# Performance work log

Measured on AMD Instinct MI355X. Metric: run time of the kernel, lower is better.

## Reference

```python
import jax, jax.numpy as jnp
import numpy as np

C = 256
CK = C // 8  # qk projection dim


def setup_inputs() -> dict:
    key = jax.random.key(0)
    ks = jax.random.split(key, 8)
    B, H, W = 4, 64, 64
    x = jax.random.normal(ks[0], (B, C, W, H), dtype=jnp.float32)
    s = 1.0 / np.sqrt(C)
    Wf = jax.random.normal(ks[1], (CK, C), dtype=jnp.float32) * s
    bf = jax.random.normal(ks[2], (CK,), dtype=jnp.float32) * 0.01
    Wg = jax.random.normal(ks[3], (CK, C), dtype=jnp.float32) * s
    bg = jax.random.normal(ks[4], (CK,), dtype=jnp.float32) * 0.01
    Wh = jax.random.normal(ks[5], (C, C), dtype=jnp.float32) * s
    bh = jax.random.normal(ks[6], (C,), dtype=jnp.float32) * 0.01
    gamma = jax.random.normal(ks[7], (1,), dtype=jnp.float32) * 0.1
    return {"x": x, "Wf": Wf, "bf": bf, "Wg": Wg, "bg": bg,
            "Wh": Wh, "bh": bh, "gamma": gamma}


def reference(x, Wf, bf, Wg, bg, Wh, bh, gamma):
    B, Cc, Wd, Hd = x.shape
    N = Wd * Hd
    xf = x.reshape(B, Cc, N)  # B C N
    # 1x1 conv1d == channel matmul
    f = jnp.einsum('oc,bcn->bon', Wf, xf) + bf[None, :, None]  # B CK N
    g = jnp.einsum('oc,bcn->bon', Wg, xf) + bg[None, :, None]  # B CK N
    h = jnp.einsum('oc,bcn->bon', Wh, xf) + bh[None, :, None]  # B C N
    # s[b,i,j] = sum_k f[b,k,i] g[b,k,j]
    s = jnp.einsum('bki,bkj->bij', f, g)  # B N N
    attention = jax.nn.softmax(s, axis=-1)
    # out[b,c,i] = sum_j h[b,c,j] attention[b,i,j]
    out = jnp.einsum('bcj,bij->bci', h, attention)  # B C N
    out = out.reshape(B, Cc, Wd, Hd)
    return gamma[0] * out + x
```

## Files before the change

kernel.cpp:

```cpp
#include <hip/hip_runtime.h>

typedef __bf16 bf16x8 __attribute__((ext_vector_type(8)));
typedef __bf16 bf16x4 __attribute__((ext_vector_type(4)));
typedef float f32x4 __attribute__((ext_vector_type(4)));
typedef float f32x16 __attribute__((ext_vector_type(16)));

__device__ __forceinline__ f32x4 mfma16(bf16x8 a, bf16x8 b, f32x4 c) {
  return __builtin_amdgcn_mfma_f32_16x16x32_bf16(a, b, c, 0, 0, 0);
}
__device__ __forceinline__ f32x16 mfma32(bf16x8 a, bf16x8 b, f32x16 c) {
  return __builtin_amdgcn_mfma_f32_32x32x16_bf16(a, b, c, 0, 0, 0);
}

__global__ void wcvt_kernel(const float* __restrict__ Wf, const float* __restrict__ Wg,
                            const float* __restrict__ Wh, __bf16* __restrict__ Wb) {
  int i = blockIdx.x * 256 + threadIdx.x;
  float v;
  if (i < 8192)       v = Wf[i];
  else if (i < 16384) v = Wg[i - 8192];
  else                v = Wh[i - 16384];
  Wb[i] = (__bf16)v;
}

__global__ __launch_bounds__(512) void proj_kernel(
    const float* __restrict__ x, const float* __restrict__ bfv,
    const float* __restrict__ bgv, const float* __restrict__ bhv,
    const __bf16* __restrict__ Wb, __bf16* __restrict__ fgT,
    __bf16* __restrict__ hb) {
  __shared__ __align__(16) char smem[2560 + 18432];
  __bf16* xT = (__bf16*)smem;
  __bf16* ho = (__bf16*)(smem + 2560);

  const int t = threadIdx.x;
  const int l = t & 63, wg = t >> 6, q = l >> 4, l15 = l & 15;
  const int nh = wg & 1, oh = wg >> 1;
  const int bi = blockIdx.x;
  const int b = bi >> 7;
  const int n0 = (bi & 127) << 5;

  const float* xb = x + (size_t)b * 256 * 4096;

  f32x4 acc[5];
#pragma unroll
  for (int i = 0; i < 5; i++) acc[i] = (f32x4){0.f, 0.f, 0.f, 0.f};

  const int c_rel = t >> 4;
  const int n2 = (t & 15) * 2;

#pragma unroll 1
  for (int kc = 0; kc < 8; kc++) {
    __syncthreads();
    float2 v = *(const float2*)(xb + (size_t)(kc * 32 + c_rel) * 4096 + n0 + n2);
    xT[(n2 + 0) * 40 + c_rel] = (__bf16)v.x;
    xT[(n2 + 1) * 40 + c_rel] = (__bf16)v.y;
    __syncthreads();
    bf16x8 af = *(const bf16x8*)(xT + (nh * 16 + l15) * 40 + q * 8);
    const __bf16* wp = Wb + (size_t)(oh * 80 + l15) * 256 + kc * 32 + q * 8;
#pragma unroll
    for (int ot = 0; ot < 5; ot++) {
      bf16x8 bfr = *(const bf16x8*)(wp + (size_t)ot * 16 * 256);
      acc[ot] = mfma16(af, bfr, acc[ot]);
    }
  }

#pragma unroll
  for (int ot = 0; ot < 5; ot++) {
    int o = oh * 80 + ot * 16 + l15;
    float bias = (o < 32) ? bfv[o] : (o < 64) ? bgv[o - 32] : bhv[o - 64];
#pragma unroll
    for (int r = 0; r < 4; r++) {
      int n_rel = nh * 16 + q * 4 + r;
      float val = acc[ot][r] + bias;
      if (o < 64) {
        fgT[((size_t)b * 4096 + n0 + n_rel) * 64 + o] = (__bf16)val;
      } else {
        ho[(o - 64) * 36 + n_rel] = (__bf16)val;
      }
    }
  }
  __syncthreads();
  unsigned short* hbu = (unsigned short*)hb + (size_t)b * 256 * 4096 + n0;
  const unsigned short* hou = (const unsigned short*)ho;
  for (int e = t; e < 4096; e += 512) {
    int c = e >> 4, nn = (e & 15) * 2;
    unsigned int vv = *(const unsigned int*)(hou + c * 36 + nn);
    *(unsigned int*)(hbu + (size_t)c * 4096 + nn) = vv;
  }
}

__global__ __launch_bounds__(256, 3) void attn_kernel(
    const __bf16* __restrict__ fgT, const __bf16* __restrict__ hb,
    __bf16* __restrict__ pO, float* __restrict__ Lp) {
  __shared__ __align__(16) char smem[35072];
  __bf16* pb0 = (__bf16*)smem;
  __bf16* pb1 = (__bf16*)(smem + 17408);
  __bf16* stage = (__bf16*)smem;
  float* Lbuf = (float*)(smem + 34816);

  const int t = threadIdx.x;
  const int l = t & 63, w = t >> 6;
  const int h = l >> 5, l31 = l & 31;

  const int bi = blockIdx.x;
  const int xcd = bi & 7, slot = bi >> 3;
  const int combo = xcd * 2 + (slot & 1);
  const int b = combo >> 2, jp = combo & 3;
  const int n0 = (slot >> 1) << 6;

  const __bf16* fgb = fgT + (size_t)b * 4096 * 64;
  const __bf16* hbb = hb + (size_t)b * 256 * 4096;
  const int jq0 = jp << 10;

  if (t < 64) Lbuf[t] = 0.f;

  const int it_s = w >> 1, jt = w & 1;

  const __bf16* qp = fgb + (size_t)(n0 + it_s * 32 + l31) * 64 + h * 8;
  const bf16x8 qf0 = *(const bf16x8*)(qp);
  const bf16x8 qf1 = *(const bf16x8*)(qp + 16);

  f32x16 acc[2][2] = {};
  float rs[16];
#pragma unroll
  for (int r = 0; r < 16; r++) rs[r] = 0.f;

  const __bf16* vbase = hbb + (size_t)(w * 64 + l31) * 4096 + h * 8;

  {
    const __bf16* kp = fgb + (size_t)(jq0 + jt * 32 + l31) * 64 + 32 + h * 8;
    bf16x8 kf0 = *(const bf16x8*)(kp);
    bf16x8 kf1 = *(const bf16x8*)(kp + 16);
    f32x16 s = {};
    s = mfma32(qf0, kf0, s);
    s = mfma32(qf1, kf1, s);
#pragma unroll
    for (int r = 0; r < 16; r++) {
      float p = __expf(s[r]);
      rs[r] += p;
      int i_loc = it_s * 32 + (r & 3) + 8 * (r >> 2) + 4 * h;
      pb0[i_loc * 136 + jt * 32 + l31] = (__bf16)p;
    }
  }
  bf16x8 vf[2][4];
#pragma unroll
  for (int ci = 0; ci < 2; ci++)
#pragma unroll
    for (int kc = 0; kc < 4; kc++)
      vf[ci][kc] = *(const bf16x8*)(vbase + (size_t)ci * 32 * 4096 + jq0 + kc * 16);
  __syncthreads();

#pragma unroll 1
  for (int it = 0; it < 16; ++it) {
    __bf16* buf = (it & 1) ? pb1 : pb0;
    __bf16* nb  = (it & 1) ? pb0 : pb1;
    const int jn = jq0 + (((it + 1) & 15) << 6);

    bf16x8 kf0, kf1;
    if (it < 15) {
      const __bf16* kp = fgb + (size_t)(jn + jt * 32 + l31) * 64 + 32 + h * 8;
      kf0 = *(const bf16x8*)(kp);
      kf1 = *(const bf16x8*)(kp + 16);
    }

#pragma unroll
    for (int kc = 0; kc < 4; kc++) {
      bf16x8 pf0 = *(const bf16x8*)(buf + (size_t)(l31) * 136 + kc * 16 + h * 8);
      bf16x8 pf1 = *(const bf16x8*)(buf + (size_t)(32 + l31) * 136 + kc * 16 + h * 8);
      acc[0][0] = mfma32(pf0, vf[0][kc], acc[0][0]);
      acc[0][1] = mfma32(pf1, vf[0][kc], acc[0][1]);
      acc[1][0] = mfma32(pf0, vf[1][kc], acc[1][0]);
      acc[1][1] = mfma32(pf1, vf[1][kc], acc[1][1]);
      vf[0][kc] = *(const bf16x8*)(vbase + jn + kc * 16);
      vf[1][kc] = *(const bf16x8*)(vbase + (size_t)32 * 4096 + jn + kc * 16);
    }

    if (it < 15) {
      f32x16 s = {};
      s = mfma32(qf0, kf0, s);
      s = mfma32(qf1, kf1, s);
#pragma unroll
      for (int r = 0; r < 16; r++) {
        float p = __expf(s[r]);
        rs[r] += p;
        int i_loc = it_s * 32 + (r & 3) + 8 * (r >> 2) + 4 * h;
        nb[i_loc * 136 + jt * 32 + l31] = (__bf16)p;
      }
    }
    __syncthreads();
  }

#pragma unroll
  for (int r = 0; r < 16; r++) {
    float s = rs[r];
    s += __shfl_xor(s, 1, 32); s += __shfl_xor(s, 2, 32);
    s += __shfl_xor(s, 4, 32); s += __shfl_xor(s, 8, 32);
    s += __shfl_xor(s, 16, 32);
    if (l31 == 0) {
      int row = it_s * 32 + (r & 3) + 8 * (r >> 2) + 4 * h;
      atomicAdd(&Lbuf[row], s);
    }
  }

#pragma unroll
  for (int ci = 0; ci < 2; ci++) {
    int c_loc = w * 64 + ci * 32 + l31;
#pragma unroll
    for (int ii = 0; ii < 2; ii++)
#pragma unroll
      for (int r = 0; r < 16; r++) {
        int i_loc = ii * 32 + (r & 3) + 8 * (r >> 2) + 4 * h;
        stage[(size_t)c_loc * 66 + i_loc] = (__bf16)acc[ci][ii][r];
      }
  }
  __syncthreads();

  unsigned short* ob = (unsigned short*)pO + (size_t)(jp * 4 + b) * 256 * 4096 + n0;
  const unsigned short* su = (const unsigned short*)stage;
#pragma unroll 1
  for (int e = t; e < 8192; e += 256) {
    int c = e >> 5, i2 = (e & 31) * 2;
    unsigned int v = *(const unsigned int*)(su + c * 66 + i2);
    *(unsigned int*)(ob + (size_t)c * 4096 + i2) = v;
  }
  if (t < 64) Lp[(size_t)(jp * 4 + b) * 4096 + n0 + t] = Lbuf[t];
}

__global__ __launch_bounds__(256) void norm_kernel(
    const float* __restrict__ x, const float* __restrict__ gamma_p,
    const __bf16* __restrict__ pO, const float* __restrict__ Lp,
    float* __restrict__ out) {
  const int bc = blockIdx.x;
  const int b = bc >> 8;
  const float gm = gamma_p[0];
  const float* xr = x + (size_t)bc * 4096;
  float* orow = out + (size_t)bc * 4096;
  const __bf16* pbase = pO + (size_t)bc * 4096;
  const float* lbase = Lp + (size_t)b * 4096;

  for (int i0 = threadIdx.x * 4; i0 < 4096; i0 += 1024) {
    float4 xv = *(const float4*)(xr + i0);
    float s0 = 0.f, s1 = 0.f, s2 = 0.f, s3 = 0.f;
    float l0 = 0.f, l1 = 0.f, l2 = 0.f, l3 = 0.f;
#pragma unroll
    for (int jp = 0; jp < 4; jp++) {
      bf16x4 pv = *(const bf16x4*)(pbase + (size_t)jp * 4194304 + i0);
      s0 += (float)pv[0]; s1 += (float)pv[1]; s2 += (float)pv[2]; s3 += (float)pv[3];
      float4 lv = *(const float4*)(lbase + (size_t)jp * 16384 + i0);
      l0 += lv.x; l1 += lv.y; l2 += lv.z; l3 += lv.w;
    }
    float4 ov;
    ov.x = gm * s0 / l0 + xv.x;
    ov.y = gm * s1 / l1 + xv.y;
    ov.z = gm * s2 / l2 + xv.z;
    ov.w = gm * s3 / l3 + xv.w;
    *(float4*)(orow + i0) = ov;
  }
}

extern "C" void kernel_launch(void* const* d_in, const int* in_sizes, int n_in,
                              void* d_out, int out_size, void* d_ws, size_t ws_size,
                              hipStream_t stream) {
  const float* x   = (const float*)d_in[0];
  const float* Wf  = (const float*)d_in[1];
  const float* bfv = (const float*)d_in[2];
  const float* Wg  = (const float*)d_in[3];
  const float* bgv = (const float*)d_in[4];
  const float* Wh  = (const float*)d_in[5];
  const float* bhv = (const float*)d_in[6];
  const float* gm  = (const float*)d_in[7];
  float* out = (float*)d_out;

  char* ws = (char*)d_ws;
  __bf16* Wb  = (__bf16*)ws;
  __bf16* fgT = (__bf16*)(ws + 262144);
  __bf16* hb  = (__bf16*)(ws + 2359296);
  __bf16* pO  = (__bf16*)(ws + 10747904);
  float*  Lp  = (float*)(ws + 44302336);

  hipLaunchKernelGGL(wcvt_kernel, dim3(320), dim3(256), 0, stream, Wf, Wg, Wh, Wb);
  hipLaunchKernelGGL(proj_kernel, dim3(512), dim3(512), 0, stream,
                     x, bfv, bgv, bhv, Wb, fgT, hb);
  hipLaunchKernelGGL(attn_kernel, dim3(1024), dim3(256), 0, stream,
                     fgT, hb, pO, Lp);
  hipLaunchKernelGGL(norm_kernel, dim3(1024), dim3(256), 0, stream,
                     x, gm, pO, Lp, out);
}
```

Before: 195.9 us.

## Pre-pack Q/K and V into MFMA fragment order for contiguous attention loads

The projection kernel now writes the Q/K and V intermediates in a blocked layout that matches the MFMA operand fragments. Each lane's 8-element bf16 load in the attention kernel then sits in a contiguous, coalesced span instead of being strided across 128-byte or 8 KB rows. This aims to cut memory transactions and cache pressure in the attention loop. The cost is more complex index arithmetic and scattered 2-byte stores in the projection epilogue, since the Q/K store pattern changes.

```diff
diff --git a/kernel.cpp b/kernel.cpp
--- a/kernel.cpp
+++ b/kernel.cpp
@@ -25,8 +25,8 @@
 __global__ __launch_bounds__(512) void proj_kernel(
     const float* __restrict__ x, const float* __restrict__ bfv,
     const float* __restrict__ bgv, const float* __restrict__ bhv,
-    const __bf16* __restrict__ Wb, __bf16* __restrict__ fgT,
-    __bf16* __restrict__ hb) {
+    const __bf16* __restrict__ Wb, __bf16* __restrict__ qkpk,
+    __bf16* __restrict__ vpk) {
   __shared__ __align__(16) char smem[2560 + 18432];
   __bf16* xT = (__bf16*)smem;
   __bf16* ho = (__bf16*)(smem + 2560);
@@ -36,7 +36,8 @@
   const int nh = wg & 1, oh = wg >> 1;
   const int bi = blockIdx.x;
   const int b = bi >> 7;
-  const int n0 = (bi & 127) << 5;
+  const int nt = bi & 127;
+  const int n0 = nt << 5;
 
   const float* xb = x + (size_t)b * 256 * 4096;
 
@@ -67,29 +68,36 @@
   for (int ot = 0; ot < 5; ot++) {
     int o = oh * 80 + ot * 16 + l15;
     float bias = (o < 32) ? bfv[o] : (o < 64) ? bgv[o - 32] : bhv[o - 64];
-#pragma unroll
-    for (int r = 0; r < 4; r++) {
-      int n_rel = nh * 16 + q * 4 + r;
-      float val = acc[ot][r] + bias;
-      if (o < 64) {
-        fgT[((size_t)b * 4096 + n0 + n_rel) * 64 + o] = (__bf16)val;
-      } else {
-        ho[(o - 64) * 36 + n_rel] = (__bf16)val;
+    if (oh == 0 && ot < 4) {
+      int qk = o >> 5, fr = (o >> 4) & 1, hh = (o >> 3) & 1, e = o & 7;
+      size_t base = ((size_t)b * 128 + nt) * 2048 + qk * 1024 + fr * 512 + hh * 256;
+#pragma unroll
+      for (int r = 0; r < 4; r++) {
+        int n_rel = nh * 16 + q * 4 + r;
+        qkpk[base + n_rel * 8 + e] = (__bf16)(acc[ot][r] + bias);
+      }
+    } else {
+#pragma unroll
+      for (int r = 0; r < 4; r++) {
+        int n_rel = nh * 16 + q * 4 + r;
+        ho[(o - 64) * 36 + n_rel] = (__bf16)(acc[ot][r] + bias);
       }
     }
   }
   __syncthreads();
-  unsigned short* hbu = (unsigned short*)hb + (size_t)b * 256 * 4096 + n0;
+  unsigned short* vpku = (unsigned short*)vpk + (size_t)b * 1048576;
   const unsigned short* hou = (const unsigned short*)ho;
   for (int e = t; e < 4096; e += 512) {
     int c = e >> 4, nn = (e & 15) * 2;
+    int n = n0 + nn;
+    int jc = n >> 4, hh = (n >> 3) & 1, ee = n & 7;
     unsigned int vv = *(const unsigned int*)(hou + c * 36 + nn);
-    *(unsigned int*)(hbu + (size_t)c * 4096 + nn) = vv;
+    *(unsigned int*)(vpku + (((size_t)(jc * 2 + hh) * 256 + c) * 8 + ee)) = vv;
   }
 }
 
 __global__ __launch_bounds__(256, 3) void attn_kernel(
-    const __bf16* __restrict__ fgT, const __bf16* __restrict__ hb,
+    const __bf16* __restrict__ qkpk, const __bf16* __restrict__ vpk,
     __bf16* __restrict__ pO, float* __restrict__ Lp) {
   __shared__ __align__(16) char smem[35072];
   __bf16* pb0 = (__bf16*)smem;
@@ -107,29 +115,29 @@
   const int b = combo >> 2, jp = combo & 3;
   const int n0 = (slot >> 1) << 6;
 
-  const __bf16* fgb = fgT + (size_t)b * 4096 * 64;
-  const __bf16* hbb = hb + (size_t)b * 256 * 4096;
+  const __bf16* qkb = qkpk + (size_t)b * 262144;
+  const __bf16* vpb = vpk + (size_t)b * 1048576;
   const int jq0 = jp << 10;
 
   if (t < 64) Lbuf[t] = 0.f;
 
   const int it_s = w >> 1, jt = w & 1;
 
-  const __bf16* qp = fgb + (size_t)(n0 + it_s * 32 + l31) * 64 + h * 8;
+  const __bf16* qp = qkb + ((n0 >> 5) + it_s) * 2048 + h * 256 + l31 * 8;
   const bf16x8 qf0 = *(const bf16x8*)(qp);
-  const bf16x8 qf1 = *(const bf16x8*)(qp + 16);
+  const bf16x8 qf1 = *(const bf16x8*)(qp + 512);
 
   f32x16 acc[2][2] = {};
   float rs[16];
 #pragma unroll
   for (int r = 0; r < 16; r++) rs[r] = 0.f;
 
-  const __bf16* vbase = hbb + (size_t)(w * 64 + l31) * 4096 + h * 8;
+  const int vco = h * 2048 + (w * 64 + l31) * 8;
 
   {
-    const __bf16* kp = fgb + (size_t)(jq0 + jt * 32 + l31) * 64 + 32 + h * 8;
+    const __bf16* kp = qkb + ((jq0 >> 5) + jt) * 2048 + 1024 + h * 256 + l31 * 8;
     bf16x8 kf0 = *(const bf16x8*)(kp);
-    bf16x8 kf1 = *(const bf16x8*)(kp + 16);
+    bf16x8 kf1 = *(const bf16x8*)(kp + 512);
     f32x16 s = {};
     s = mfma32(qf0, kf0, s);
     s = mfma32(qf1, kf1, s);
@@ -146,20 +154,20 @@
   for (int ci = 0; ci < 2; ci++)
 #pragma unroll
     for (int kc = 0; kc < 4; kc++)
-      vf[ci][kc] = *(const bf16x8*)(vbase + (size_t)ci * 32 * 4096 + jq0 + kc * 16);
+      vf[ci][kc] = *(const bf16x8*)(vpb + (size_t)((jq0 >> 4) + kc) * 4096 + vco + ci * 256);
   __syncthreads();
 
 #pragma unroll 1
   for (int it = 0; it < 16; ++it) {
     __bf16* buf = (it & 1) ? pb1 : pb0;
     __bf16* nb  = (it & 1) ? pb0 : pb1;
-    const int jn = jq0 + (((it + 1) & 15) << 6);
+    const int jn4 = (jq0 >> 4) + (((it + 1) & 15) << 2);
 
     bf16x8 kf0, kf1;
     if (it < 15) {
-      const __bf16* kp = fgb + (size_t)(jn + jt * 32 + l31) * 64 + 32 + h * 8;
+      const __bf16* kp = qkb + ((jn4 >> 1) + jt) * 2048 + 1024 + h * 256 + l31 * 8;
       kf0 = *(const bf16x8*)(kp);
-      kf1 = *(const bf16x8*)(kp + 16);
+      kf1 = *(const bf16x8*)(kp + 512);
     }
 
 #pragma unroll
@@ -170,8 +178,8 @@
       acc[0][1] = mfma32(pf1, vf[0][kc], acc[0][1]);
       acc[1][0] = mfma32(pf0, vf[1][kc], acc[1][0]);
       acc[1][1] = mfma32(pf1, vf[1][kc], acc[1][1]);
-      vf[0][kc] = *(const bf16x8*)(vbase + jn + kc * 16);
-      vf[1][kc] = *(const bf16x8*)(vbase + (size_t)32 * 4096 + jn + kc * 16);
+      vf[0][kc] = *(const bf16x8*)(vpb + (size_t)(jn4 + kc) * 4096 + vco);
+      vf[1][kc] = *(const bf16x8*)(vpb + (size_t)(jn4 + kc) * 4096 + vco + 256);
     }
 
     if (it < 15) {
@@ -271,17 +279,17 @@
   float* out = (float*)d_out;
 
   char* ws = (char*)d_ws;
-  __bf16* Wb  = (__bf16*)ws;
-  __bf16* fgT = (__bf16*)(ws + 262144);
-  __bf16* hb  = (__bf16*)(ws + 2359296);
-  __bf16* pO  = (__bf16*)(ws + 10747904);
-  float*  Lp  = (float*)(ws + 44302336);
+  __bf16* Wb   = (__bf16*)ws;
+  __bf16* qkpk = (__bf16*)(ws + 262144);
+  __bf16* vpk  = (__bf16*)(ws + 2359296);
+  __bf16* pO   = (__bf16*)(ws + 10747904);
+  float*  Lp   = (float*)(ws + 44302336);
 
   hipLaunchKernelGGL(wcvt_kernel, dim3(320), dim3(256), 0, stream, Wf, Wg, Wh, Wb);
   hipLaunchKernelGGL(proj_kernel, dim3(512), dim3(512), 0, stream,
-                     x, bfv, bgv, bhv, Wb, fgT, hb);
+                     x, bfv, bgv, bhv, Wb, qkpk, vpk);
   hipLaunchKernelGGL(attn_kernel, dim3(1024), dim3(256), 0, stream,
-                     fgT, hb, pO, Lp);
+                     qkpk, vpk, pO, Lp);
   hipLaunchKernelGGL(norm_kernel, dim3(1024), dim3(256), 0, stream,
                      x, gm, pO, Lp, out);
 }
```

After: 162.3 us. 1.21x faster.
